# Optimization experiments

Measured on AMD Instinct MI355X. Metric: run time of the kernel, lower is better.

The kernel has to match this reference:

```python
import jax, jax.numpy as jnp
import numpy as np

# Dims: N batch, I input channels, C = in/hidden/attention/projection/out channels (all 128),
# streams=1, groups=1, spatial kernel 3, dropout 0.
N, I, C, H, W = 8, 128, 128, 36, 36


def _conv(x, w, pad):
    # x: [N, Cin, H, W], w: [Cout, Cin, kh, kw]
    return jax.lax.conv_general_dilated(
        x, w, (1, 1), pad, dimension_numbers=("NCHW", "OIHW", "NCHW"))


def _bias(b):
    return b[None, :, None, None]


def setup_inputs() -> dict:
    key = jax.random.key(0)
    ks = jax.random.split(key, 16)
    std = 0.05

    def w(k, o, i, s):
        return jax.random.normal(k, (o, i, s, s), jnp.float32) * std

    p = {}
    p["inp"] = jax.random.normal(ks[0], (N, I, H, W), jnp.float32)
    p["c0"] = jax.random.normal(ks[1], (1, C, 1, 1), jnp.float32)
    # proj_x: 1x1 conv input->in_channels, bias init 0
    p["w_x"] = w(ks[2], C, I, 1)
    p["b_x"] = jnp.zeros((C,), jnp.float32)
    # token convs (3x3, no bias); q uses SAME pad, k/v VALID
    p["w_qx"] = w(ks[3], C, C, 3)
    p["w_qc"] = w(ks[4], C, C, 3)
    scale = C ** (-0.5)  # gain = attn_channels^-0.5 on k projections
    p["w_kx"] = w(ks[5], C, C, 3) * scale
    p["w_kc"] = w(ks[6], C, C, 3) * scale
    p["w_vx"] = w(ks[7], C, C, 3)
    p["w_vc"] = w(ks[8], C, C, 3)
    # gating 1x1 convs: proj_z (bias=init_gate=1), proj_n (bias=0), in 2*proj channels
    p["w_z"] = w(ks[9], C, 2 * C, 1)
    p["b_z"] = jnp.ones((C,), jnp.float32)
    p["w_n"] = w(ks[10], C, 2 * C, 1)
    p["b_n"] = jnp.zeros((C,), jnp.float32)
    # proj_h: in_channels + 2*projection_channels -> hidden
    p["w_h"] = w(ks[11], C, 3 * C, 1)
    p["b_h"] = jnp.zeros((C,), jnp.float32)
    # output 1x1 conv hidden -> out_channels
    p["w_o"] = w(ks[12], C, C, 1)
    p["b_o"] = jnp.zeros((C,), jnp.float32)
    return p


def reference(inp, c0, w_x, b_x, w_qx, w_qc, w_kx, w_kc, w_vx, w_vc,
              w_z, b_z, w_n, b_n, w_h, b_h, w_o, b_o):
    # proj_x (1x1) -> x: [N, C, H, W]
    x = _conv(inp, w_x, "VALID") + _bias(b_x)
    n_, _, hh, ww = x.shape
    c = jnp.broadcast_to(c0, (n_, c0.shape[1], hh, ww))
    q_len = hh * ww
    # q: SAME pad -> Q = H*W tokens; k/v: VALID -> D = (H-2)*(W-2) tokens
    q = jnp.stack([_conv(x, w_qx, "SAME"), _conv(c, w_qc, "SAME")], 0)
    q = q.reshape(2, n_, -1, q_len)                      # [A, N, C, Q]
    k_x = _conv(x, w_kx, "VALID")
    d_len = k_x.shape[2] * k_x.shape[3]
    k = jnp.stack([k_x, _conv(c, w_kc, "VALID")], 0).reshape(2, n_, -1, d_len)   # [B, N, C, D]
    v = jnp.stack([_conv(x, w_vx, "VALID"), _conv(c, w_vc, "VALID")], 0)
    v = v.reshape(2, n_, -1, d_len)                      # [B, N, C, D]
    # all (A query source) x (B key/value source) attention pairs
    attn = jax.nn.softmax(jnp.einsum("ancq,bncd->anbqd", q, k), axis=-1)
    a = jnp.einsum("bncd,anbqd->anbcq", v, attn)         # [A, N, B, C, Q]
    a = a.reshape(2, n_, -1, hh, ww)                     # channels = B*C = 2*proj
    a_x, a_c = a[0], a[1]
    # GRU-style gated cell update (stored state; not part of the returned output)
    z = jax.nn.sigmoid(_conv(a_c, w_z, "VALID") + _bias(b_z))
    n_cand = jnp.tanh(_conv(a_c, w_n, "VALID") + _bias(b_n))
    c_new = z * c + (1.0 - z) * n_cand  # noqa: F841 (past['c'] in the original)
    # hidden: tanh(proj_h(cat[x, a_x])), dropout p=0 is identity
    xa = jnp.concatenate([x, a_x], axis=1)               # [N, 3*C, H, W]
    h = jnp.tanh(_conv(xa, w_h, "VALID") + _bias(b_h))
    return _conv(h, w_o, "VALID") + _bias(b_o)           # [N, C, H, W]
```

## Files before the change

### kernel.cpp

```cpp
#include <hip/hip_runtime.h>
#include <hip/hip_bf16.h>
#include <math.h>

#define NN 8
#define CH 128
#define HH 36
#define WWI 36
#define PP 1296
#define DD 1156
#define VP 1280
#define KC 1152
#define QT 81
#define DT 5
#define XPP 1444

typedef __attribute__((ext_vector_type(8))) short short8;
typedef __attribute__((ext_vector_type(4))) float f32x4;
typedef __attribute__((ext_vector_type(8))) _Float16 half8;

__device__ inline unsigned short f2bf(float f) {
    __hip_bfloat16 h = __float2bfloat16(f);
    return __builtin_bit_cast(unsigned short, h);
}
__device__ inline float fast_tanh(float x) {
    float e = __expf(2.f * x);
    return 1.f - 2.f / (e + 1.f);
}
#define MFMA(a, b, c) __builtin_amdgcn_mfma_f32_16x16x32_bf16((a), (b), (c), 0, 0, 0)
#define GLDS(g, l) __builtin_amdgcn_global_load_lds( \
    (const __attribute__((address_space(1))) unsigned int*)(g), \
    (__attribute__((address_space(3))) unsigned int*)(l), 16, 0, 0)

__global__ __launch_bounds__(256)
void k_setup(const float* __restrict__ wq, const float* __restrict__ wk,
             const float* __restrict__ wv, const float* __restrict__ wh,
             const float* __restrict__ wo, const float* __restrict__ wx,
             const float* __restrict__ c0, const float* __restrict__ w_vc,
             const float* __restrict__ b_h,
             unsigned short* __restrict__ wcat, unsigned short* __restrict__ whb,
             unsigned short* __restrict__ wob,
             float* __restrict__ hconst,
             const float* __restrict__ inp, const float* __restrict__ bx,
             unsigned short* __restrict__ xp)
{
    if (blockIdx.x >= 901) {
        const int n = blockIdx.x - 901;
        unsigned short* xpn = xp + (size_t)n * XPP * CH;
        for (int b = threadIdx.x; b < 148 * 16; b += 256) {
            int cell = b >> 4, part = b & 15;
            int y, x;
            if (cell < 38)       { y = 0;              x = cell; }
            else if (cell < 76)  { y = 37;             x = cell - 38; }
            else if (cell < 112) { y = cell - 76 + 1;  x = 0; }
            else                 { y = cell - 112 + 1; x = 37; }
            *(uint4*)&xpn[((size_t)(y * 38 + x)) * CH + part * 8] = make_uint4(0, 0, 0, 0);
        }
        return;
    }
    if (blockIdx.x >= 577) {
        const int t = threadIdx.x;
        const int wave = t >> 6, lane = t & 63;
        const int pid = (blockIdx.x - 577) * 4 + wave;
        const int n = pid / 162;
        const int rem = pid - n * 162;
        const int by = rem / 81;
        const int qg = rem - by * 81;
        const int quad = lane >> 4, lrow = lane & 15;
        const int p0 = qg * 16;
        const int co0 = by * 64;
        const float* in_n = inp + (size_t)n * CH * PP;
        f32x4 acc[4] = {};

#pragma unroll
        for (int ks = 0; ks < 4; ++ks) {
            union { short8 v; unsigned short u[8]; } a;
            int ci0 = ks * 32 + quad * 8;
#pragma unroll
            for (int j = 0; j < 8; ++j)
                a.u[j] = f2bf(in_n[(size_t)(ci0 + j) * PP + p0 + lrow]);
#pragma unroll
            for (int ni = 0; ni < 4; ++ni) {
                const float* wrow = wx + (size_t)(co0 + ni * 16 + lrow) * CH + ks * 32 + quad * 8;
                float4 f0 = *(const float4*)wrow;
                float4 f1 = *(const float4*)(wrow + 4);
                union { short8 v; unsigned short u[8]; } b;
                b.u[0] = f2bf(f0.x); b.u[1] = f2bf(f0.y);
                b.u[2] = f2bf(f0.z); b.u[3] = f2bf(f0.w);
                b.u[4] = f2bf(f1.x); b.u[5] = f2bf(f1.y);
                b.u[6] = f2bf(f1.z); b.u[7] = f2bf(f1.w);
                acc[ni] = MFMA(a.v, b.v, acc[ni]);
            }
        }
        unsigned short* xn = xp + (size_t)n * XPP * CH;
#pragma unroll
        for (int ni = 0; ni < 4; ++ni) {
            float bv = bx[co0 + ni * 16 + lrow];
#pragma unroll
            for (int r = 0; r < 4; ++r) {
                int p = p0 + quad * 4 + r;
                int off = ((p / 36 + 1) * 38 + (p % 36) + 1) * CH;
                xn[(size_t)off + co0 + ni * 16 + lrow] = f2bf(acc[ni][r] + bv);
            }
        }
        return;
    }
    if (blockIdx.x == 576) {
        __shared__ float c0s[CH];
        __shared__ float part[256];
        __shared__ float vcs[CH];
        const int t = threadIdx.x;
        const int c = t & 127, half = t >> 7;
        if (t < CH) c0s[t] = c0[t];
        __syncthreads();
        {
            const float* row = w_vc + (size_t)c * 1152 + half * 576;
            float s = 0.f;
#pragma unroll 4
            for (int j4 = 0; j4 < 144; ++j4) {
                float4 v = ((const float4*)row)[j4];
                int j = half * 576 + j4 * 4;
                s += v.x * c0s[j / 9] + v.y * c0s[(j + 1) / 9]
                   + v.z * c0s[(j + 2) / 9] + v.w * c0s[(j + 3) / 9];
            }
            part[t] = s;
        }
        __syncthreads();
        if (t < CH) vcs[t] = part[t] + part[t + 128];
        __syncthreads();
        {
            const float* wrow = wh + (size_t)c * 384 + 256 + half * 64;
            float hs = 0.f;
#pragma unroll
            for (int j4 = 0; j4 < 16; ++j4) {
                float4 v = ((const float4*)wrow)[j4];
                int ci = half * 64 + j4 * 4;
                hs += v.x * vcs[ci] + v.y * vcs[ci + 1] + v.z * vcs[ci + 2] + v.w * vcs[ci + 3];
            }
            part[t] = hs;
        }
        __syncthreads();
        if (t < CH) hconst[t] = b_h[t] + part[t] + part[t + 128];
        return;
    }
    int t = blockIdx.x * 256 + threadIdx.x;
    int co = t / KC;
    int rem = t - co * KC;
    int tap = rem >> 7, ci = rem & 127;
    int iidx = co * KC + ci * 9 + tap;
    wcat[t] = f2bf(wq[iidx]);
    wcat[147456 + t] = f2bf(wk[iidx]);
    wcat[294912 + t] = f2bf(wv[iidx]);
    if (t < 32768) {
        int c2 = t >> 8, k2 = t & 255;
        whb[t] = f2bf(wh[c2 * 384 + k2]);
    }
    if (t < 16384) wob[t] = f2bf(wo[t]);
}

__global__ __launch_bounds__(256)
void k_conv(const unsigned short* __restrict__ xp, const unsigned short* __restrict__ wcat,
            unsigned short* __restrict__ qt, unsigned short* __restrict__ kt,
            unsigned short* __restrict__ vb)
{
    __shared__ unsigned short lA[3][2048];
    __shared__ unsigned short lB[3][4096];
    const int t = threadIdx.x;
    const int wave = t >> 6, lane = t & 63;
    const int quad = lane >> 4, lrow = lane & 15;
    const int mode = blockIdx.y;
    const int n = blockIdx.z;
    const int limit = (mode == 0) ? PP : DD;
    const int tile0 = blockIdx.x * 64;
    if (tile0 >= limit) return;
    const unsigned short* xn = xp + (size_t)n * XPP * CH;
    const unsigned short* wb = wcat + (size_t)mode * 128 * KC;

    const int aseg = t & 3;
    int apr, apc;
    {
        int tok = tile0 + (t >> 2); if (tok >= limit) tok = limit - 1;
        int dv = (mode == 0) ? 36 : 34;
        apr = tok / dv; apc = tok - apr * dv;
        if (mode != 0) { apr += 1; apc += 1; }
    }
    const unsigned short* wbr0 = wb + (size_t)(wave * 16 + (lane >> 2)) * KC + (lane & 3) * 8;
    const unsigned short* wbr1 = wb + (size_t)(64 + wave * 16 + (lane >> 2)) * KC + (lane & 3) * 8;
    const int ldsA = wave * 512;
    const int ldsB0 = wave * 512;
    const int ldsB1 = 2048 + wave * 512;

    auto stage = [&](int ks, int buf) {
        int tap = ks >> 2;
        int ky = tap / 3, kx = tap - ky * 3;
        int ci = (ks & 3) * 32 + aseg * 8;
        const unsigned short* srcA = xn + ((size_t)((apr + ky) * 38 + apc + kx)) * CH + ci;
        int koff = tap * 128 + (ks & 3) * 32;
        GLDS(srcA, &lA[buf][ldsA]);
        GLDS(wbr0 + koff, &lB[buf][ldsB0]);
        GLDS(wbr1 + koff, &lB[buf][ldsB1]);
    };

    f32x4 acc[4][2] = {};
    stage(0, 0);
    stage(1, 1);
    stage(2, 2);

#pragma unroll
    for (int ks = 0; ks < 36; ++ks) {
        if (ks < 34)      asm volatile("s_waitcnt vmcnt(6)" ::: "memory");
        else if (ks == 34) asm volatile("s_waitcnt vmcnt(3)" ::: "memory");
        else               asm volatile("s_waitcnt vmcnt(0)" ::: "memory");
        __builtin_amdgcn_sched_barrier(0);
        __builtin_amdgcn_s_barrier();
        __builtin_amdgcn_sched_barrier(0);
        const int buf = ks % 3;
        short8 b0 = *(const short8*)&lB[buf][(wave * 32 + lrow) * 32 + quad * 8];
        short8 b1 = *(const short8*)&lB[buf][(wave * 32 + 16 + lrow) * 32 + quad * 8];
#pragma unroll
        for (int mi = 0; mi < 4; ++mi) {
            short8 a = *(const short8*)&lA[buf][(mi * 16 + lrow) * 32 + quad * 8];
            acc[mi][0] = MFMA(a, b0, acc[mi][0]);
            acc[mi][1] = MFMA(a, b1, acc[mi][1]);
        }
        __builtin_amdgcn_sched_barrier(0);
        __builtin_amdgcn_s_barrier();
        __builtin_amdgcn_sched_barrier(0);
        if (ks < 33) stage(ks + 3, buf);
    }

    if (mode == 0) {
        unsigned short* qn = qt + (size_t)n * PP * CH;
#pragma unroll
        for (int mi = 0; mi < 4; ++mi)
#pragma unroll
            for (int r = 0; r < 4; ++r) {
                int p = tile0 + mi * 16 + quad * 4 + r;
                if (p < PP)
#pragma unroll
                    for (int ni = 0; ni < 2; ++ni)
                        qn[(size_t)p * CH + (wave * 2 + ni) * 16 + lrow] = f2bf(acc[mi][ni][r]);
            }
    } else if (mode == 1) {
        unsigned short* kn = kt + (size_t)n * DD * CH;
#pragma unroll
        for (int mi = 0; mi < 4; ++mi)
#pragma unroll
            for (int r = 0; r < 4; ++r) {
                int d = tile0 + mi * 16 + quad * 4 + r;
                if (d < DD)
#pragma unroll
                    for (int ni = 0; ni < 2; ++ni)
                        kn[(size_t)d * CH + (wave * 2 + ni) * 16 + lrow] = f2bf(acc[mi][ni][r]);
            }
    } else {
        unsigned short* vn = vb + (size_t)n * CH * VP;
#pragma unroll
        for (int mi = 0; mi < 4; ++mi)
#pragma unroll
            for (int r = 0; r < 4; ++r) {
                int d = tile0 + mi * 16 + quad * 4 + r;
                if (d < DD)
#pragma unroll
                    for (int ni = 0; ni < 2; ++ni)
                        vn[(size_t)((wave * 2 + ni) * 16 + lrow) * VP + d] = f2bf(acc[mi][ni][r]);
            }
    }
}

__global__ __launch_bounds__(256)
void k_attn(const unsigned short* __restrict__ qt, const unsigned short* __restrict__ kt,
            const unsigned short* __restrict__ vb, _Float16* __restrict__ po,
            float* __restrict__ pm, float* __restrict__ pl)
{
    __shared__ unsigned short lS[2][128 * 40];
    __shared__ unsigned short lp[4][16 * 136];
    const int t = threadIdx.x;
    const int wave = t >> 6, lane = t & 63;
    const int quad = lane >> 4, lrow = lane & 15;
    const int qg = blockIdx.x;
    const int dt = blockIdx.y;
    const int n = blockIdx.z;
    const int qti = qg * 4 + wave;
    const int d0 = dt * 256;
    const unsigned short* qn = qt + (size_t)n * PP * CH;
    const unsigned short* kn = kt + (size_t)n * DD * CH;
    const unsigned short* vn = vb + (size_t)n * CH * VP;

    const int arow = t >> 2, aseg8 = (t & 3) * 8;
    const int lo0 = arow * 40 + aseg8;
    const int lo1 = (arow + 64) * 40 + aseg8;

    short8 qa[4];
    {
        int qrow = qti * 16 + lrow; if (qrow >= PP) qrow = PP - 1;
#pragma unroll
        for (int ks = 0; ks < 4; ++ks)
            qa[ks] = *(const short8*)&qn[(size_t)qrow * CH + ks * 32 + quad * 8];
    }

    f32x4 o[8] = {};
    float mx[4] = {-1e30f, -1e30f, -1e30f, -1e30f};
    float rs[4] = {0.f, 0.f, 0.f, 0.f};

#pragma unroll
    for (int h = 0; h < 2; ++h) {
        const int dbase = d0 + h * 128;
        int kr0 = dbase + arow;      if (kr0 >= DD) kr0 = DD - 1;
        int kr1 = dbase + arow + 64; if (kr1 >= DD) kr1 = DD - 1;
        const unsigned short* kp0 = kn + (size_t)kr0 * CH + aseg8;
        const unsigned short* kp1 = kn + (size_t)kr1 * CH + aseg8;
        const unsigned short* vp0 = vn + (size_t)arow * VP + dbase + aseg8;
        const unsigned short* vp1 = vn + (size_t)(arow + 64) * VP + dbase + aseg8;

        f32x4 s[8] = {};
        uint4 r0 = *(const uint4*)kp0;
        uint4 r1 = *(const uint4*)kp1;
        *(uint4*)&lS[0][lo0] = r0;
        *(uint4*)&lS[0][lo1] = r1;
        __syncthreads();
#pragma unroll
        for (int ks = 0; ks < 4; ++ks) {
            const int buf = ks & 1;
            if (ks < 3) {
                r0 = *(const uint4*)(kp0 + (ks + 1) * 32);
                r1 = *(const uint4*)(kp1 + (ks + 1) * 32);
            }
#pragma unroll
            for (int ni = 0; ni < 8; ++ni) {
                short8 b = *(const short8*)&lS[buf][(ni * 16 + lrow) * 40 + quad * 8];
                s[ni] = MFMA(qa[ks], b, s[ni]);
            }
            if (ks < 3) {
                *(uint4*)&lS[buf ^ 1][lo0] = r0;
                *(uint4*)&lS[buf ^ 1][lo1] = r1;
            }
            __syncthreads();
        }

#pragma unroll
        for (int ni = 0; ni < 8; ++ni)
            if (dbase + ni * 16 + lrow >= DD)
#pragma unroll
                for (int r = 0; r < 4; ++r) s[ni][r] = -1e30f;

        float hm[4] = {-1e30f, -1e30f, -1e30f, -1e30f};
#pragma unroll
        for (int ni = 0; ni < 8; ++ni)
#pragma unroll
            for (int r = 0; r < 4; ++r) hm[r] = fmaxf(hm[r], s[ni][r]);
#pragma unroll
        for (int off = 1; off < 16; off <<= 1)
#pragma unroll
            for (int r = 0; r < 4; ++r) hm[r] = fmaxf(hm[r], __shfl_xor(hm[r], off, 64));

        float m[4], sc[4];
#pragma unroll
        for (int r = 0; r < 4; ++r) {
            m[r] = fmaxf(mx[r], hm[r]);
            sc[r] = __expf(mx[r] - m[r]);
        }

        float hs[4] = {0.f, 0.f, 0.f, 0.f};
#pragma unroll
        for (int ni = 0; ni < 8; ++ni)
#pragma unroll
            for (int r = 0; r < 4; ++r) {
                float e = __expf(s[ni][r] - m[r]);
                s[ni][r] = e;
                hs[r] += e;
            }
#pragma unroll
        for (int off = 1; off < 16; off <<= 1)
#pragma unroll
            for (int r = 0; r < 4; ++r) hs[r] += __shfl_xor(hs[r], off, 64);
#pragma unroll
        for (int r = 0; r < 4; ++r) {
            rs[r] = rs[r] * sc[r] + hs[r];
            mx[r] = m[r];
        }
#pragma unroll
        for (int ni = 0; ni < 8; ++ni)
#pragma unroll
            for (int r = 0; r < 4; ++r) o[ni][r] *= sc[r];

#pragma unroll
        for (int ni = 0; ni < 8; ++ni)
#pragma unroll
            for (int r = 0; r < 4; ++r)
                lp[wave][(quad * 4 + r) * 136 + ni * 16 + lrow] = f2bf(s[ni][r]);

        r0 = *(const uint4*)vp0;
        r1 = *(const uint4*)vp1;
        *(uint4*)&lS[0][lo0] = r0;
        *(uint4*)&lS[0][lo1] = r1;
        __syncthreads();
#pragma unroll
        for (int ks = 0; ks < 4; ++ks) {
            const int buf = ks & 1;
            if (ks < 3) {
                r0 = *(const uint4*)(vp0 + (ks + 1) * 32);
                r1 = *(const uint4*)(vp1 + (ks + 1) * 32);
            }
            short8 pa = *(const short8*)&lp[wave][lrow * 136 + ks * 32 + quad * 8];
#pragma unroll
            for (int ni = 0; ni < 8; ++ni) {
                short8 b = *(const short8*)&lS[buf][(ni * 16 + lrow) * 40 + quad * 8];
                o[ni] = MFMA(pa, b, o[ni]);
            }
            if (ks < 3) {
                *(uint4*)&lS[buf ^ 1][lo0] = r0;
                *(uint4*)&lS[buf ^ 1][lo1] = r1;
            }
            __syncthreads();
        }
    }

    if (qti < QT) {
        const int base = (n * QT + qti) * DT + dt;
        _Float16* pob = po + (size_t)base * 2048;
#pragma unroll
        for (int ni = 0; ni < 8; ++ni)
#pragma unroll
            for (int r = 0; r < 4; ++r)
                pob[(quad * 4 + r) * 128 + ni * 16 + lrow] = (_Float16)o[ni][r];
        if (lrow == 0)
#pragma unroll
            for (int r = 0; r < 4; ++r) {
                pm[base * 16 + quad * 4 + r] = mx[r];
                pl[base * 16 + quad * 4 + r] = rs[r];
            }
    }
}

__global__ __launch_bounds__(256)
void k_ahout(const _Float16* __restrict__ po, const float* __restrict__ pm,
             const float* __restrict__ pl, const unsigned short* __restrict__ xp,
             const unsigned short* __restrict__ whb, const float* __restrict__ hconst,
             const unsigned short* __restrict__ wob, const float* __restrict__ bo,
             float* __restrict__ out)
{
    __shared__ float sm[80], ssc[80], smg[16], sli[16];
    __shared__ unsigned short la0[16 * 136];
    __shared__ unsigned short lh[16 * 136];
    const int qti = blockIdx.x;
    const int n = blockIdx.y;
    const int base = (n * QT + qti) * DT;
    const int t = threadIdx.x;

    if (t < 80) sm[t] = pm[base * 16 + t];
    __syncthreads();
    if (t < 16) {
        float mg = -1e30f;
#pragma unroll
        for (int dt = 0; dt < DT; ++dt) mg = fmaxf(mg, sm[dt * 16 + t]);
        float ls = 0.f;
#pragma unroll
        for (int dt = 0; dt < DT; ++dt) ls += __expf(sm[dt * 16 + t] - mg) * pl[base * 16 + dt * 16 + t];
        smg[t] = mg; sli[t] = 1.f / ls;
    }
    __syncthreads();
    if (t < 80) ssc[t] = __expf(sm[t] - smg[t & 15]);
    __syncthreads();
    {
        const int row = t >> 4;
        const int c0 = (t & 15) * 8;
        float acc[8] = {};
#pragma unroll
        for (int dt = 0; dt < DT; ++dt) {
            half8 v = *(const half8*)&po[(size_t)(base + dt) * 2048 + t * 8];
            float scv = ssc[dt * 16 + row];
#pragma unroll
            for (int j = 0; j < 8; ++j) acc[j] += scv * (float)v[j];
        }
        float inv = sli[row];
#pragma unroll
        for (int j = 0; j < 8; ++j)
            la0[row * 136 + c0 + j] = f2bf(acc[j] * inv);
    }
    __syncthreads();

    const int wave = t >> 6, lane = t & 63;
    const int quad = lane >> 4, lrow = lane & 15;
    const int p0 = qti * 16;
    const unsigned short* x0 = xp + (size_t)n * XPP * CH;
    const int ptok = p0 + lrow;
    const int xoff = ((ptok / 36 + 1) * 38 + (ptok % 36) + 1) * CH;

    f32x4 acc1[2] = {};
#pragma unroll
    for (int ks = 0; ks < 8; ++ks) {
        int col = (ks & 3) * 32 + quad * 8;
        short8 a;
        if (ks < 4) a = *(const short8*)&x0[(size_t)xoff + col];
        else        a = *(const short8*)&la0[lrow * 136 + col];
#pragma unroll
        for (int j = 0; j < 2; ++j) {
            int ni = wave * 2 + j;
            short8 b = *(const short8*)&whb[(size_t)(ni * 16 + lrow) * 256 + ks * 32 + quad * 8];
            acc1[j] = MFMA(a, b, acc1[j]);
        }
    }
#pragma unroll
    for (int j = 0; j < 2; ++j) {
        int ni = wave * 2 + j;
        float hc = hconst[ni * 16 + lrow];
#pragma unroll
        for (int r = 0; r < 4; ++r)
            lh[(quad * 4 + r) * 136 + ni * 16 + lrow] = f2bf(fast_tanh(acc1[j][r] + hc));
    }
    __syncthreads();

    f32x4 acc2[2] = {};
#pragma unroll
    for (int ks = 0; ks < 4; ++ks) {
        short8 a = *(const short8*)&lh[lrow * 136 + ks * 32 + quad * 8];
#pragma unroll
        for (int j = 0; j < 2; ++j) {
            int ni = wave * 2 + j;
            short8 b = *(const short8*)&wob[(size_t)(ni * 16 + lrow) * CH + ks * 32 + quad * 8];
            acc2[j] = MFMA(a, b, acc2[j]);
        }
    }
#pragma unroll
    for (int j = 0; j < 2; ++j) {
        int ni = wave * 2 + j;
        float bv = bo[ni * 16 + lrow];
#pragma unroll
        for (int r = 0; r < 4; ++r)
            out[((size_t)(n * CH + ni * 16 + lrow)) * PP + p0 + quad * 4 + r] = acc2[j][r] + bv;
    }
}

extern "C" void kernel_launch(void* const* d_in, const int* in_sizes, int n_in,
                              void* d_out, int out_size, void* d_ws, size_t ws_size,
                              hipStream_t stream)
{
    const float* inp  = (const float*)d_in[0];
    const float* c0   = (const float*)d_in[1];
    const float* w_x  = (const float*)d_in[2];
    const float* b_x  = (const float*)d_in[3];
    const float* w_qx = (const float*)d_in[4];
    const float* w_kx = (const float*)d_in[6];
    const float* w_vx = (const float*)d_in[8];
    const float* w_vc = (const float*)d_in[9];
    const float* w_h  = (const float*)d_in[14];
    const float* b_h  = (const float*)d_in[15];
    const float* w_o  = (const float*)d_in[16];
    const float* b_o  = (const float*)d_in[17];
    float* out = (float*)d_out;

    char* w = (char*)d_ws;
    unsigned short* xp   = (unsigned short*)(w);
    unsigned short* qt   = (unsigned short*)(w + 2957312);
    unsigned short* kt   = (unsigned short*)(w + 5611520);
    unsigned short* vb   = (unsigned short*)(w + 7979008);
    unsigned short* wcat = (unsigned short*)(w + 10600448);
    unsigned short* whb  = (unsigned short*)(w + 11485184);
    unsigned short* wob  = (unsigned short*)(w + 11550720);
    float* hconst        = (float*)(w + 11583488);
    float* pm            = (float*)(w + 11616256);
    float* pl            = (float*)(w + 11824128);
    _Float16* po         = (_Float16*)(w + 12031488);

    hipLaunchKernelGGL(k_setup, dim3(909), dim3(256), 0, stream,
                       w_qx, w_kx, w_vx, w_h, w_o, w_x, c0, w_vc, b_h,
                       wcat, whb, wob, hconst, inp, b_x, xp);

    hipLaunchKernelGGL(k_conv, dim3(21, 3, NN), dim3(256), 0, stream, xp, wcat, qt, kt, vb);

    hipLaunchKernelGGL(k_attn, dim3(21, DT, NN), dim3(256), 0, stream, qt, kt, vb, po, pm, pl);

    hipLaunchKernelGGL(k_ahout, dim3(QT, NN), dim3(256), 0, stream,
                       po, pm, pl, xp, whb, hconst, wob, b_o, out);
}
```

Before: 182.8 us.

## Stream K/V tiles with direct global-to-LDS loads in a two-deep ring

```diff
diff --git a/kernel.cpp b/kernel.cpp
--- a/kernel.cpp
+++ b/kernel.cpp
@@ -272,7 +272,7 @@
             const unsigned short* __restrict__ vb, _Float16* __restrict__ po,
             float* __restrict__ pm, float* __restrict__ pl)
 {
-    __shared__ unsigned short lS[2][128 * 40];
+    __shared__ unsigned short ring[2][4096];
     __shared__ unsigned short lp[4][16 * 136];
     const int t = threadIdx.x;
     const int wave = t >> 6, lane = t & 63;
@@ -286,9 +286,26 @@
     const unsigned short* kn = kt + (size_t)n * DD * CH;
     const unsigned short* vn = vb + (size_t)n * CH * VP;
 
-    const int arow = t >> 2, aseg8 = (t & 3) * 8;
-    const int lo0 = arow * 40 + aseg8;
-    const int lo1 = (arow + 64) * 40 + aseg8;
+    const int lrow4 = lane >> 2;
+    const int lseg = lane & 3;
+
+    auto stage = [&](int c) {
+        const int h = c >> 3, k = c & 3, isV = (c >> 2) & 1;
+        const int dbase = d0 + h * 128;
+        const int buf = c & 1;
+#pragma unroll
+        for (int j = 0; j < 2; ++j) {
+            const int rowc = j * 64 + wave * 16 + lrow4;
+            const unsigned short* src;
+            if (!isV) {
+                int row = dbase + rowc; if (row >= DD) row = DD - 1;
+                src = kn + (size_t)row * CH + k * 32 + lseg * 8;
+            } else {
+                src = vn + (size_t)rowc * VP + dbase + k * 32 + lseg * 8;
+            }
+            GLDS(src, &ring[buf][j * 2048 + wave * 512]);
+        }
+    };
 
     short8 qa[4];
     {
@@ -302,39 +319,31 @@
     float mx[4] = {-1e30f, -1e30f, -1e30f, -1e30f};
     float rs[4] = {0.f, 0.f, 0.f, 0.f};
 
+    stage(0);
+    stage(1);
+
 #pragma unroll
     for (int h = 0; h < 2; ++h) {
         const int dbase = d0 + h * 128;
-        int kr0 = dbase + arow;      if (kr0 >= DD) kr0 = DD - 1;
-        int kr1 = dbase + arow + 64; if (kr1 >= DD) kr1 = DD - 1;
-        const unsigned short* kp0 = kn + (size_t)kr0 * CH + aseg8;
-        const unsigned short* kp1 = kn + (size_t)kr1 * CH + aseg8;
-        const unsigned short* vp0 = vn + (size_t)arow * VP + dbase + aseg8;
-        const unsigned short* vp1 = vn + (size_t)(arow + 64) * VP + dbase + aseg8;
-
         f32x4 s[8] = {};
-        uint4 r0 = *(const uint4*)kp0;
-        uint4 r1 = *(const uint4*)kp1;
-        *(uint4*)&lS[0][lo0] = r0;
-        *(uint4*)&lS[0][lo1] = r1;
-        __syncthreads();
-#pragma unroll
-        for (int ks = 0; ks < 4; ++ks) {
-            const int buf = ks & 1;
-            if (ks < 3) {
-                r0 = *(const uint4*)(kp0 + (ks + 1) * 32);
-                r1 = *(const uint4*)(kp1 + (ks + 1) * 32);
-            }
+
+#pragma unroll
+        for (int k = 0; k < 4; ++k) {
+            const int c = h * 8 + k;
+            asm volatile("s_waitcnt vmcnt(2)" ::: "memory");
+            __builtin_amdgcn_sched_barrier(0);
+            __builtin_amdgcn_s_barrier();
+            __builtin_amdgcn_sched_barrier(0);
+            const int buf = c & 1;
 #pragma unroll
             for (int ni = 0; ni < 8; ++ni) {
-                short8 b = *(const short8*)&lS[buf][(ni * 16 + lrow) * 40 + quad * 8];
-                s[ni] = MFMA(qa[ks], b, s[ni]);
-            }
-            if (ks < 3) {
-                *(uint4*)&lS[buf ^ 1][lo0] = r0;
-                *(uint4*)&lS[buf ^ 1][lo1] = r1;
-            }
-            __syncthreads();
+                short8 b = *(const short8*)&ring[buf][(ni * 16 + lrow) * 32 + quad * 8];
+                s[ni] = MFMA(qa[k], b, s[ni]);
+            }
+            __builtin_amdgcn_sched_barrier(0);
+            __builtin_amdgcn_s_barrier();
+            __builtin_amdgcn_sched_barrier(0);
+            stage(c + 2);
         }
 
 #pragma unroll
@@ -389,29 +398,25 @@
             for (int r = 0; r < 4; ++r)
                 lp[wave][(quad * 4 + r) * 136 + ni * 16 + lrow] = f2bf(s[ni][r]);
 
-        r0 = *(const uint4*)vp0;
-        r1 = *(const uint4*)vp1;
-        *(uint4*)&lS[0][lo0] = r0;
-        *(uint4*)&lS[0][lo1] = r1;
-        __syncthreads();
-#pragma unroll
-        for (int ks = 0; ks < 4; ++ks) {
-            const int buf = ks & 1;
-            if (ks < 3) {
-                r0 = *(const uint4*)(vp0 + (ks + 1) * 32);
-                r1 = *(const uint4*)(vp1 + (ks + 1) * 32);
-            }
-            short8 pa = *(const short8*)&lp[wave][lrow * 136 + ks * 32 + quad * 8];
+#pragma unroll
+        for (int k = 0; k < 4; ++k) {
+            const int c = h * 8 + 4 + k;
+            if (c == 15) asm volatile("s_waitcnt vmcnt(0)" ::: "memory");
+            else         asm volatile("s_waitcnt vmcnt(2)" ::: "memory");
+            __builtin_amdgcn_sched_barrier(0);
+            __builtin_amdgcn_s_barrier();
+            __builtin_amdgcn_sched_barrier(0);
+            const int buf = c & 1;
+            short8 pa = *(const short8*)&lp[wave][lrow * 136 + k * 32 + quad * 8];
 #pragma unroll
             for (int ni = 0; ni < 8; ++ni) {
-                short8 b = *(const short8*)&lS[buf][(ni * 16 + lrow) * 40 + quad * 8];
+                short8 b = *(const short8*)&ring[buf][(ni * 16 + lrow) * 32 + quad * 8];
                 o[ni] = MFMA(pa, b, o[ni]);
             }
-            if (ks < 3) {
-                *(uint4*)&lS[buf ^ 1][lo0] = r0;
-                *(uint4*)&lS[buf ^ 1][lo1] = r1;
-            }
-            __syncthreads();
+            __builtin_amdgcn_sched_barrier(0);
+            __builtin_amdgcn_s_barrier();
+            __builtin_amdgcn_sched_barrier(0);
+            if (c + 2 < 16) stage(c + 2);
         }
     }
 
```

After: 198.7 us. 1.09x slower.
